# Optimization experiments

Measured on AMD Instinct MI355X. Metric: run time of the kernel, lower is better.

The kernel has to match this reference:

```python
import jax, jax.numpy as jnp
import numpy as np

B, T, D, H = 4, 2048, 1024, 16
DK = D // H

def setup_inputs() -> dict:
    key = jax.random.key(0)
    k1, k2, k3 = jax.random.split(key, 3)
    x = jax.random.normal(k1, (B, T, D), dtype=jnp.float32)
    w_qkv = jax.random.normal(k2, (D, 3 * D), dtype=jnp.float32) * (1.0 / np.sqrt(D))
    w_proj = jax.random.normal(k3, (D, D), dtype=jnp.float32) * (1.0 / np.sqrt(D))
    # additive causal mask: 0 on/below diagonal, -inf above
    neg = jnp.finfo(jnp.float32).min
    attn_mask = jnp.where(jnp.tril(jnp.ones((T, T), dtype=bool)), 0.0, neg)[None, None]
    return {"x": x, "attn_mask": attn_mask, "w_qkv": w_qkv, "w_proj": w_proj}


def reference(x, attn_mask, w_qkv, w_proj):
    Bx, Tx, Dx = x.shape
    qkv = x @ w_qkv                                  # [B,T,3D]
    q, k, v = jnp.split(qkv, 3, axis=-1)
    # [B,T,D] -> [B,H,T,dk]
    def to_heads(t):
        return t.reshape(Bx, Tx, H, DK).transpose(0, 2, 1, 3)
    q, k, v = to_heads(q), to_heads(k), to_heads(v)
    attn = jnp.einsum("bhqd,bhkd->bhqk", q, k) / jnp.sqrt(jnp.float32(DK))
    attn = attn + attn_mask
    attn = jax.nn.softmax(attn, axis=-1)
    out = jnp.einsum("bhqk,bhkd->bhqd", attn, v)     # [B,H,T,dk]
    out = out.transpose(0, 2, 1, 3).reshape(Bx, Tx, Dx)
    return out @ w_proj
```

## Files before the change

### kernel.cpp

```cpp
#include <hip/hip_runtime.h>
#include <hip/hip_bf16.h>
#include <stdint.h>

typedef __bf16 bf16x8 __attribute__((ext_vector_type(8)));
typedef __bf16 bf16x4 __attribute__((ext_vector_type(4)));
typedef float  f32x4  __attribute__((ext_vector_type(4)));

__device__ __forceinline__ void gl_lds16(const void* g, void* l) {
  __builtin_amdgcn_global_load_lds(
      (const __attribute__((address_space(1))) unsigned int*)g,
      (__attribute__((address_space(3))) unsigned int*)l, 16, 0, 0);
}

__global__ __launch_bounds__(256) void convert_x(
    const float* __restrict__ src, __bf16* __restrict__ dst) {
  const size_t i = ((size_t)blockIdx.x * 256 + threadIdx.x) * 8;
  float4 v0 = *reinterpret_cast<const float4*>(src + i);
  float4 v1 = *reinterpret_cast<const float4*>(src + i + 4);
  bf16x8 o;
  o[0] = (__bf16)v0.x; o[1] = (__bf16)v0.y; o[2] = (__bf16)v0.z; o[3] = (__bf16)v0.w;
  o[4] = (__bf16)v1.x; o[5] = (__bf16)v1.y; o[6] = (__bf16)v1.z; o[7] = (__bf16)v1.w;
  *reinterpret_cast<bf16x8*>(dst + i) = o;
}

__global__ __launch_bounds__(256) void transpose_convert(
    const float* __restrict__ src, __bf16* __restrict__ dst, int K, int N) {
  __shared__ __bf16 tile[64][65];
  const int n0 = blockIdx.x * 64, k0 = blockIdx.y * 64;
  const int t = threadIdx.x;
#pragma unroll
  for (int e = 0; e < 16; ++e) {
    int idx = e * 256 + t;
    int kk = idx >> 6, nn = idx & 63;
    tile[nn][kk] = (__bf16)src[(size_t)(k0 + kk) * N + n0 + nn];
  }
  __syncthreads();
#pragma unroll
  for (int e = 0; e < 16; ++e) {
    int idx = e * 256 + t;
    int nn = idx >> 6, kk = idx & 63;
    dst[(size_t)(n0 + nn) * K + k0 + kk] = tile[nn][kk];
  }
}

__global__ __launch_bounds__(256) void qkv_gemm(
    const __bf16* __restrict__ Xb, const __bf16* __restrict__ WT,
    __bf16* __restrict__ Qb, __bf16* __restrict__ Kb, __bf16* __restrict__ Vb) {
  __shared__ __bf16 As[128 * 32];
  __shared__ __bf16 Bs[128 * 32];
  const int t = threadIdx.x;
  const int l = t & 63, w = t >> 6;
  const int g = l >> 4, lr = l & 15;
  const int wm = w >> 1, wn = w & 1;
  const int lin = blockIdx.y * gridDim.x + blockIdx.x;
  const int cpx = (gridDim.x * gridDim.y) >> 3;
  const int swz = (lin & 7) * cpx + (lin >> 3);
  const int m0 = (swz / 24) * 128, n0 = (swz % 24) * 128;

  f32x4 acc[4][4] = {};

  for (int kb = 0; kb < 1024; kb += 32) {
#pragma unroll
    for (int rep = 0; rep < 2; ++rep) {
      int c = w * 128 + rep * 64 + l;
      int row = c >> 2, col = (c & 3) * 8;
      gl_lds16(Xb + (size_t)(m0 + row) * 1024 + kb + col,
               As + (size_t)(w * 128 + rep * 64) * 8);
      gl_lds16(WT + (size_t)(n0 + row) * 1024 + kb + col,
               Bs + (size_t)(w * 128 + rep * 64) * 8);
    }
    __syncthreads();

    bf16x8 a[4], b[4];
#pragma unroll
    for (int mf = 0; mf < 4; ++mf)
      a[mf] = *reinterpret_cast<bf16x8*>(&As[(wm * 64 + mf * 16 + lr) * 32 + g * 8]);
#pragma unroll
    for (int nf = 0; nf < 4; ++nf)
      b[nf] = *reinterpret_cast<bf16x8*>(&Bs[(wn * 64 + nf * 16 + lr) * 32 + g * 8]);
#pragma unroll
    for (int mf = 0; mf < 4; ++mf)
#pragma unroll
      for (int nf = 0; nf < 4; ++nf)
        acc[mf][nf] = __builtin_amdgcn_mfma_f32_16x16x32_bf16(
            a[mf], b[nf], acc[mf][nf], 0, 0, 0);
    __syncthreads();
  }

#pragma unroll
  for (int mf = 0; mf < 4; ++mf)
#pragma unroll
    for (int nf = 0; nf < 4; ++nf) {
      int m_ = m0 + wm * 64 + mf * 16 + g * 4;
      int n = n0 + wn * 64 + nf * 16 + lr;
      int which = n >> 10, hc = n & 1023;
      int hh = hc >> 6, dk = hc & 63;
      int bbv = m_ >> 11, tt = m_ & 2047;
      if (which == 2) {
        bf16x4 vk;
        vk[0] = (__bf16)acc[mf][nf][0]; vk[1] = (__bf16)acc[mf][nf][1];
        vk[2] = (__bf16)acc[mf][nf][2]; vk[3] = (__bf16)acc[mf][nf][3];
        *reinterpret_cast<bf16x4*>(
            &Vb[((size_t)(bbv * 16 + hh) * 64 + dk) * 2048 + tt]) = vk;
      } else {
#pragma unroll
        for (int j = 0; j < 4; ++j) {
          size_t off = (((size_t)(bbv * 16 + hh)) * 2048 + tt + j) * 64 + dk;
          float v = acc[mf][nf][j];
          if (which == 0) Qb[off] = (__bf16)(v * 0.18033688f);
          else            Kb[off] = (__bf16)v;
        }
      }
    }
}

__global__ __launch_bounds__(256, 2) void attn_kernel(
    const __bf16* __restrict__ Qb, const __bf16* __restrict__ Kb,
    const __bf16* __restrict__ VTb, __bf16* __restrict__ Ob) {
  __shared__ __bf16 Ks[2][4096];
  __shared__ __bf16 Vs[2][4096];
  __shared__ __bf16 PlA[4][1024];
  __shared__ __bf16 PlB[4][1024];
  const int t = threadIdx.x, l = t & 63, w = t >> 6;
  const int g = l >> 4, lr = l & 15;
  const int bid = blockIdx.x;
  const int logical = (bid & 7) * 64 + (bid >> 3);
  const int pj = logical & 7, bh = logical >> 3;
  const int bb = bh >> 4, h = bh & 15;
  const __bf16* Kbase = Kb  + (size_t)bh * 2048 * 64;
  const __bf16* Vbase = VTb + (size_t)bh * 64 * 2048;
  const __bf16* Qbase = Qb  + (size_t)bh * 2048 * 64;
  const int swz = (lr & 7) << 4;

  int cur = 0;
#pragma unroll 1
  for (int phase = 0; phase < 2; ++phase) {
    const int J = phase ? (15 - pj) : pj;
    const int qtA = 2 * J, qtB = 2 * J + 1;
    const int qrowA = J * 128 + w * 16 + lr;
    const int qrowB = qrowA + 64;
    const bf16x8 qfA0 = *reinterpret_cast<const bf16x8*>(Qbase + (size_t)qrowA * 64 + g * 8);
    const bf16x8 qfA1 = *reinterpret_cast<const bf16x8*>(Qbase + (size_t)qrowA * 64 + 32 + g * 8);
    const bf16x8 qfB0 = *reinterpret_cast<const bf16x8*>(Qbase + (size_t)qrowB * 64 + g * 8);
    const bf16x8 qfB1 = *reinterpret_cast<const bf16x8*>(Qbase + (size_t)qrowB * 64 + 32 + g * 8);

    f32x4 otA[4] = {}, otB[4] = {};
    float lsA = 0.f, lsB = 0.f;

#pragma unroll
    for (int rep = 0; rep < 2; ++rep) {
      int c = w * 128 + rep * 64 + l;
      int row = c >> 3, cc = c & 7;
      int pc = (cc ^ (row & 7)) * 8;
      gl_lds16(Kbase + (size_t)row * 64 + pc, &Ks[cur][(w * 128 + rep * 64) * 8]);
      gl_lds16(Vbase + (size_t)row * 2048 + pc, &Vs[cur][(w * 128 + rep * 64) * 8]);
    }
    __syncthreads();

    for (int kt = 0; kt <= qtB; ++kt) {
      const bool aAct = (kt <= qtA);
      if (kt < qtB) {
        const int nv0 = (kt + 1) * 64;
#pragma unroll
        for (int rep = 0; rep < 2; ++rep) {
          int c = w * 128 + rep * 64 + l;
          int row = c >> 3, cc = c & 7;
          int pc = (cc ^ (row & 7)) * 8;
          gl_lds16(Kbase + (size_t)(nv0 + row) * 64 + pc,
                   &Ks[cur ^ 1][(w * 128 + rep * 64) * 8]);
          gl_lds16(Vbase + (size_t)row * 2048 + nv0 + pc,
                   &Vs[cur ^ 1][(w * 128 + rep * 64) * 8]);
        }
      }
      bf16x8 klo[4], khi[4];
#pragma unroll
      for (int nf = 0; nf < 4; ++nf) {
        const char* kr = (const char*)&Ks[cur][(nf * 16 + lr) * 64];
        klo[nf] = *reinterpret_cast<const bf16x8*>(kr + ((g * 16) ^ swz));
        khi[nf] = *reinterpret_cast<const bf16x8*>(kr + ((64 + g * 16) ^ swz));
      }
      f32x4 stA[4], stB[4];
      __builtin_amdgcn_s_setprio(1);
#pragma unroll
      for (int nf = 0; nf < 4; ++nf) {
        f32x4 z = {};
        z = __builtin_amdgcn_mfma_f32_16x16x32_bf16(klo[nf], qfB0, z, 0, 0, 0);
        stB[nf] = __builtin_amdgcn_mfma_f32_16x16x32_bf16(khi[nf], qfB1, z, 0, 0, 0);
      }
      if (aAct) {
#pragma unroll
        for (int nf = 0; nf < 4; ++nf) {
          f32x4 z = {};
          z = __builtin_amdgcn_mfma_f32_16x16x32_bf16(klo[nf], qfA0, z, 0, 0, 0);
          stA[nf] = __builtin_amdgcn_mfma_f32_16x16x32_bf16(khi[nf], qfA1, z, 0, 0, 0);
        }
      }
      __builtin_amdgcn_s_setprio(0);
      if (kt == qtB) {
#pragma unroll
        for (int nf = 0; nf < 4; ++nf)
#pragma unroll
          for (int j = 0; j < 4; ++j)
            if (nf * 16 + g * 4 + j > w * 16 + lr) stB[nf][j] = -INFINITY;
      }
      if (aAct && kt == qtA) {
#pragma unroll
        for (int nf = 0; nf < 4; ++nf)
#pragma unroll
          for (int j = 0; j < 4; ++j)
            if (nf * 16 + g * 4 + j > w * 16 + lr) stA[nf][j] = -INFINITY;
      }
      {
        float rs = 0.f;
        char* prow = (char*)&PlB[w][lr * 64];
#pragma unroll
        for (int nf = 0; nf < 4; ++nf) {
#pragma unroll
          for (int j = 0; j < 4; ++j) {
            float p = __builtin_amdgcn_exp2f(stB[nf][j]);
            stB[nf][j] = p;
            rs += p;
          }
          bf16x4 pk;
          pk[0] = (__bf16)stB[nf][0]; pk[1] = (__bf16)stB[nf][1];
          pk[2] = (__bf16)stB[nf][2]; pk[3] = (__bf16)stB[nf][3];
          *reinterpret_cast<bf16x4*>(prow + ((nf * 32 + g * 8) ^ swz)) = pk;
        }
        lsB += rs;
      }
      if (aAct) {
        float rs = 0.f;
        char* prow = (char*)&PlA[w][lr * 64];
#pragma unroll
        for (int nf = 0; nf < 4; ++nf) {
#pragma unroll
          for (int j = 0; j < 4; ++j) {
            float p = __builtin_amdgcn_exp2f(stA[nf][j]);
            stA[nf][j] = p;
            rs += p;
          }
          bf16x4 pk;
          pk[0] = (__bf16)stA[nf][0]; pk[1] = (__bf16)stA[nf][1];
          pk[2] = (__bf16)stA[nf][2]; pk[3] = (__bf16)stA[nf][3];
          *reinterpret_cast<bf16x4*>(prow + ((nf * 32 + g * 8) ^ swz)) = pk;
        }
        lsA += rs;
      }
      {
        bf16x8 vlo[4], vhi[4];
#pragma unroll
        for (int nf = 0; nf < 4; ++nf) {
          const char* vr = (const char*)&Vs[cur][(nf * 16 + lr) * 64];
          vlo[nf] = *reinterpret_cast<const bf16x8*>(vr + ((g * 16) ^ swz));
          vhi[nf] = *reinterpret_cast<const bf16x8*>(vr + ((64 + g * 16) ^ swz));
        }
        const char* prB = (const char*)&PlB[w][lr * 64];
        bf16x8 pb0 = *reinterpret_cast<const bf16x8*>(prB + ((g * 16) ^ swz));
        bf16x8 pb1 = *reinterpret_cast<const bf16x8*>(prB + ((64 + g * 16) ^ swz));
        __builtin_amdgcn_s_setprio(1);
#pragma unroll
        for (int nf = 0; nf < 4; ++nf) {
          otB[nf] = __builtin_amdgcn_mfma_f32_16x16x32_bf16(vlo[nf], pb0, otB[nf], 0, 0, 0);
          otB[nf] = __builtin_amdgcn_mfma_f32_16x16x32_bf16(vhi[nf], pb1, otB[nf], 0, 0, 0);
        }
        __builtin_amdgcn_s_setprio(0);
        if (aAct) {
          const char* prA = (const char*)&PlA[w][lr * 64];
          bf16x8 pa0 = *reinterpret_cast<const bf16x8*>(prA + ((g * 16) ^ swz));
          bf16x8 pa1 = *reinterpret_cast<const bf16x8*>(prA + ((64 + g * 16) ^ swz));
          __builtin_amdgcn_s_setprio(1);
#pragma unroll
          for (int nf = 0; nf < 4; ++nf) {
            otA[nf] = __builtin_amdgcn_mfma_f32_16x16x32_bf16(vlo[nf], pa0, otA[nf], 0, 0, 0);
            otA[nf] = __builtin_amdgcn_mfma_f32_16x16x32_bf16(vhi[nf], pa1, otA[nf], 0, 0, 0);
          }
          __builtin_amdgcn_s_setprio(0);
        }
      }
      __syncthreads();
      cur ^= 1;
    }

    lsA += __shfl_xor(lsA, 16); lsA += __shfl_xor(lsA, 32);
    lsB += __shfl_xor(lsB, 16); lsB += __shfl_xor(lsB, 32);
    const float rlA = 1.f / lsA, rlB = 1.f / lsB;
#pragma unroll
    for (int nf = 0; nf < 4; ++nf) {
      bf16x4 ok;
      ok[0] = (__bf16)(otA[nf][0] * rlA); ok[1] = (__bf16)(otA[nf][1] * rlA);
      ok[2] = (__bf16)(otA[nf][2] * rlA); ok[3] = (__bf16)(otA[nf][3] * rlA);
      *reinterpret_cast<bf16x4*>(
          &Ob[((size_t)(bb * 2048 + qrowA)) * 1024 + h * 64 + nf * 16 + g * 4]) = ok;
      bf16x4 ok2;
      ok2[0] = (__bf16)(otB[nf][0] * rlB); ok2[1] = (__bf16)(otB[nf][1] * rlB);
      ok2[2] = (__bf16)(otB[nf][2] * rlB); ok2[3] = (__bf16)(otB[nf][3] * rlB);
      *reinterpret_cast<bf16x4*>(
          &Ob[((size_t)(bb * 2048 + qrowB)) * 1024 + h * 64 + nf * 16 + g * 4]) = ok2;
    }
  }
}

__global__ __launch_bounds__(256) void proj_gemm(
    const __bf16* __restrict__ A, const __bf16* __restrict__ WT,
    float* __restrict__ Out) {
  __shared__ __bf16 As[128 * 32];
  __shared__ __bf16 Bs[128 * 32];
  const int t = threadIdx.x;
  const int l = t & 63, w = t >> 6;
  const int g = l >> 4, lr = l & 15;
  const int wm = w >> 1, wn = w & 1;
  const int lin = blockIdx.y * gridDim.x + blockIdx.x;
  const int cpx = (gridDim.x * gridDim.y) >> 3;
  const int swz = (lin & 7) * cpx + (lin >> 3);
  const int m0 = (swz >> 3) * 128, n0 = (swz & 7) * 128;

  f32x4 acc[4][4] = {};

  for (int kb = 0; kb < 1024; kb += 32) {
#pragma unroll
    for (int rep = 0; rep < 2; ++rep) {
      int c = w * 128 + rep * 64 + l;
      int row = c >> 2, col = (c & 3) * 8;
      gl_lds16(A + (size_t)(m0 + row) * 1024 + kb + col,
               As + (size_t)(w * 128 + rep * 64) * 8);
      gl_lds16(WT + (size_t)(n0 + row) * 1024 + kb + col,
               Bs + (size_t)(w * 128 + rep * 64) * 8);
    }
    __syncthreads();

    bf16x8 a[4], b[4];
#pragma unroll
    for (int mf = 0; mf < 4; ++mf)
      a[mf] = *reinterpret_cast<bf16x8*>(&As[(wm * 64 + mf * 16 + lr) * 32 + g * 8]);
#pragma unroll
    for (int nf = 0; nf < 4; ++nf)
      b[nf] = *reinterpret_cast<bf16x8*>(&Bs[(wn * 64 + nf * 16 + lr) * 32 + g * 8]);
#pragma unroll
    for (int mf = 0; mf < 4; ++mf)
#pragma unroll
      for (int nf = 0; nf < 4; ++nf)
        acc[mf][nf] = __builtin_amdgcn_mfma_f32_16x16x32_bf16(
            a[mf], b[nf], acc[mf][nf], 0, 0, 0);
    __syncthreads();
  }

#pragma unroll
  for (int mf = 0; mf < 4; ++mf)
#pragma unroll
    for (int nf = 0; nf < 4; ++nf)
#pragma unroll
      for (int j = 0; j < 4; ++j) {
        int m = m0 + wm * 64 + mf * 16 + g * 4 + j;
        int n = n0 + wn * 64 + nf * 16 + lr;
        Out[(size_t)m * 1024 + n] = acc[mf][nf][j];
      }
}

extern "C" void kernel_launch(void* const* d_in, const int* in_sizes, int n_in,
                              void* d_out, int out_size, void* d_ws, size_t ws_size,
                              hipStream_t stream) {
  const float* x      = (const float*)d_in[0];
  const float* w_qkv  = (const float*)d_in[2];
  const float* w_proj = (const float*)d_in[3];
  float* out = (float*)d_out;

  char* ws = (char*)d_ws;
  __bf16* wt_qkv  = (__bf16*)(ws);
  __bf16* wt_proj = (__bf16*)(ws + 6291456);
  __bf16* Qb      = (__bf16*)(ws + 8388608);
  __bf16* Kb      = (__bf16*)(ws + 8388608 + 16777216);
  __bf16* VTb     = (__bf16*)(ws + 8388608 + 2 * 16777216);
  __bf16* Ob      = (__bf16*)(ws + 8388608 + 3 * 16777216);
  __bf16* Xb      = Ob;

  convert_x<<<4096, 256, 0, stream>>>(x, Xb);
  transpose_convert<<<dim3(3072 / 64, 1024 / 64), 256, 0, stream>>>(w_qkv, wt_qkv, 1024, 3072);
  transpose_convert<<<dim3(1024 / 64, 1024 / 64), 256, 0, stream>>>(w_proj, wt_proj, 1024, 1024);
  qkv_gemm<<<dim3(24, 64), 256, 0, stream>>>(Xb, wt_qkv, Qb, Kb, VTb);
  attn_kernel<<<512, 256, 0, stream>>>(Qb, Kb, VTb, Ob);
  proj_gemm<<<dim3(8, 64), 256, 0, stream>>>(Ob, wt_proj, out);
}
```

Baseline: 172.6 us.

## Rewrite QKV and projection GEMMs with shared triple-buffered swizzled 128x256 core

Replaces both GEMM kernels with a shared core that uses 128x256 tiles, a three-stage LDS ring of async global-to-LDS loads with explicit vmcnt waits and one barrier per K step, and XOR-swizzled LDS columns to avoid bank conflicts. Each wave now computes a 128x64 strip, and MFMA issue priority is raised. The aim is to hide global load latency and cut barrier and LDS-conflict overhead, at the cost of more registers and LDS per block and fewer blocks in the grid.

```diff
diff --git a/kernel.cpp b/kernel.cpp
--- a/kernel.cpp
+++ b/kernel.cpp
@@ -43,74 +43,158 @@
   }
 }
 
-__global__ __launch_bounds__(256) void qkv_gemm(
-    const __bf16* __restrict__ Xb, const __bf16* __restrict__ WT,
-    __bf16* __restrict__ Qb, __bf16* __restrict__ Kb, __bf16* __restrict__ Vb) {
-  __shared__ __bf16 As[128 * 32];
-  __shared__ __bf16 Bs[128 * 32];
-  const int t = threadIdx.x;
-  const int l = t & 63, w = t >> 6;
-  const int g = l >> 4, lr = l & 15;
-  const int wm = w >> 1, wn = w & 1;
-  const int lin = blockIdx.y * gridDim.x + blockIdx.x;
-  const int cpx = (gridDim.x * gridDim.y) >> 3;
-  const int swz = (lin & 7) * cpx + (lin >> 3);
-  const int m0 = (swz / 24) * 128, n0 = (swz % 24) * 128;
-
-  f32x4 acc[4][4] = {};
-
-  for (int kb = 0; kb < 1024; kb += 32) {
-#pragma unroll
-    for (int rep = 0; rep < 2; ++rep) {
-      int c = w * 128 + rep * 64 + l;
-      int row = c >> 2, col = (c & 3) * 8;
-      gl_lds16(Xb + (size_t)(m0 + row) * 1024 + kb + col,
-               As + (size_t)(w * 128 + rep * 64) * 8);
-      gl_lds16(WT + (size_t)(n0 + row) * 1024 + kb + col,
-               Bs + (size_t)(w * 128 + rep * 64) * 8);
-    }
-    __syncthreads();
-
-    bf16x8 a[4], b[4];
-#pragma unroll
-    for (int mf = 0; mf < 4; ++mf)
-      a[mf] = *reinterpret_cast<bf16x8*>(&As[(wm * 64 + mf * 16 + lr) * 32 + g * 8]);
+__device__ __forceinline__ void gemm_core_1024(
+    const __bf16* __restrict__ Ag, const __bf16* __restrict__ Bg,
+    int m0, int n0, __bf16* lds, f32x4 (&acc)[8][4]) {
+  const int tid = threadIdx.x;
+  const int wv = tid >> 6, l = tid & 63, g = l >> 4, lr = l & 15;
+  const int sswL = (lr & 3) ^ ((lr >> 2) & 3);
+
+  int arow[2], acol[2], brow[4], bcol[4];
+#pragma unroll
+  for (int e = 0; e < 2; ++e) {
+    int c = e * 256 + tid, row = c >> 2, slot = c & 3;
+    arow[e] = row;
+    acol[e] = (slot ^ ((row & 3) ^ ((row >> 2) & 3))) * 8;
+  }
+#pragma unroll
+  for (int e = 0; e < 4; ++e) {
+    int c = e * 256 + tid, row = c >> 2, slot = c & 3;
+    brow[e] = row;
+    bcol[e] = (slot ^ ((row & 3) ^ ((row >> 2) & 3))) * 8;
+  }
+
+  auto STAGE = [&](int bufb, int t) {
+    const int kb = t * 32;
+#pragma unroll
+    for (int e = 0; e < 2; ++e)
+      gl_lds16(Ag + (size_t)(m0 + arow[e]) * 1024 + kb + acol[e],
+               lds + bufb + (e * 256 + wv * 64) * 8);
+#pragma unroll
+    for (int e = 0; e < 4; ++e)
+      gl_lds16(Bg + (size_t)(n0 + brow[e]) * 1024 + kb + bcol[e],
+               lds + bufb + 4096 + (e * 256 + wv * 64) * 8);
+  };
+
+  int cur = 0, nx = 12288, nn = 24576;
+  STAGE(cur, 0);
+  STAGE(nx, 1);
+
+#pragma unroll 1
+  for (int t = 0; t < 32; ++t) {
+    if (t < 31) asm volatile("s_waitcnt vmcnt(6)" ::: "memory");
+    else        asm volatile("s_waitcnt vmcnt(0)" ::: "memory");
+    __builtin_amdgcn_s_barrier();
+    __builtin_amdgcn_sched_barrier(0);
+    if (t + 2 < 32) STAGE(nn, t + 2);
+
+    const char* Ab = (const char*)(lds + cur);
+    const char* Bb = (const char*)(lds + cur + 4096);
+    bf16x8 a[8], b[4];
+#pragma unroll
+    for (int mf = 0; mf < 8; ++mf)
+      a[mf] = *reinterpret_cast<const bf16x8*>(
+          Ab + (mf * 16 + lr) * 64 + ((g ^ sswL) << 4));
 #pragma unroll
     for (int nf = 0; nf < 4; ++nf)
-      b[nf] = *reinterpret_cast<bf16x8*>(&Bs[(wn * 64 + nf * 16 + lr) * 32 + g * 8]);
-#pragma unroll
-    for (int mf = 0; mf < 4; ++mf)
+      b[nf] = *reinterpret_cast<const bf16x8*>(
+          Bb + (wv * 64 + nf * 16 + lr) * 64 + ((g ^ sswL) << 4));
+    __builtin_amdgcn_s_setprio(1);
+#pragma unroll
+    for (int mf = 0; mf < 8; ++mf)
 #pragma unroll
       for (int nf = 0; nf < 4; ++nf)
         acc[mf][nf] = __builtin_amdgcn_mfma_f32_16x16x32_bf16(
             a[mf], b[nf], acc[mf][nf], 0, 0, 0);
-    __syncthreads();
-  }
-
-#pragma unroll
-  for (int mf = 0; mf < 4; ++mf)
-#pragma unroll
-    for (int nf = 0; nf < 4; ++nf) {
-      int m_ = m0 + wm * 64 + mf * 16 + g * 4;
-      int n = n0 + wn * 64 + nf * 16 + lr;
-      int which = n >> 10, hc = n & 1023;
-      int hh = hc >> 6, dk = hc & 63;
-      int bbv = m_ >> 11, tt = m_ & 2047;
-      if (which == 2) {
+    __builtin_amdgcn_s_setprio(0);
+
+    int tmp = cur; cur = nx; nx = nn; nn = tmp;
+  }
+}
+
+__global__ __launch_bounds__(256, 2) void qkv_gemm(
+    const __bf16* __restrict__ Xb, const __bf16* __restrict__ WT,
+    __bf16* __restrict__ Qb, __bf16* __restrict__ Kb, __bf16* __restrict__ Vb) {
+  __shared__ __bf16 lds[36864];
+  const int lin = blockIdx.x;
+  const int sw = (lin & 7) * 96 + (lin >> 3);
+  const int rb = sw / 12, cb = sw % 12;
+  const int m0 = rb * 128, n0 = cb * 256;
+
+  f32x4 acc[8][4] = {};
+  gemm_core_1024(Xb, WT, m0, n0, lds, acc);
+
+  const int tid = threadIdx.x, wv = tid >> 6, l = tid & 63, g = l >> 4, lr = l & 15;
+  const int which = cb >> 2;
+
+  if (which == 2) {
+#pragma unroll
+    for (int mf = 0; mf < 8; ++mf)
+#pragma unroll
+      for (int nf = 0; nf < 4; ++nf) {
+        int m_ = m0 + mf * 16 + g * 4;
+        int n  = n0 + wv * 64 + nf * 16 + lr;
+        int hc = n & 1023, hh = hc >> 6, dk = hc & 63;
+        int bbv = m_ >> 11, tt = m_ & 2047;
         bf16x4 vk;
         vk[0] = (__bf16)acc[mf][nf][0]; vk[1] = (__bf16)acc[mf][nf][1];
         vk[2] = (__bf16)acc[mf][nf][2]; vk[3] = (__bf16)acc[mf][nf][3];
         *reinterpret_cast<bf16x4*>(
             &Vb[((size_t)(bbv * 16 + hh) * 64 + dk) * 2048 + tt]) = vk;
-      } else {
-#pragma unroll
-        for (int j = 0; j < 4; ++j) {
-          size_t off = (((size_t)(bbv * 16 + hh)) * 2048 + tt + j) * 64 + dk;
-          float v = acc[mf][nf][j];
-          if (which == 0) Qb[off] = (__bf16)(v * 0.18033688f);
-          else            Kb[off] = (__bf16)v;
-        }
-      }
+      }
+  } else if (which == 0) {
+#pragma unroll
+    for (int mf = 0; mf < 8; ++mf)
+#pragma unroll
+      for (int nf = 0; nf < 4; ++nf) {
+        int m_ = m0 + mf * 16 + g * 4;
+        int n  = n0 + wv * 64 + nf * 16 + lr;
+        int hc = n & 1023, hh = hc >> 6, dk = hc & 63;
+        int bbv = m_ >> 11, tt = m_ & 2047;
+#pragma unroll
+        for (int j = 0; j < 4; ++j)
+          Qb[(((size_t)(bbv * 16 + hh)) * 2048 + tt + j) * 64 + dk] =
+              (__bf16)(acc[mf][nf][j] * 0.18033688f);
+      }
+  } else {
+#pragma unroll
+    for (int mf = 0; mf < 8; ++mf)
+#pragma unroll
+      for (int nf = 0; nf < 4; ++nf) {
+        int m_ = m0 + mf * 16 + g * 4;
+        int n  = n0 + wv * 64 + nf * 16 + lr;
+        int hc = n & 1023, hh = hc >> 6, dk = hc & 63;
+        int bbv = m_ >> 11, tt = m_ & 2047;
+#pragma unroll
+        for (int j = 0; j < 4; ++j)
+          Kb[(((size_t)(bbv * 16 + hh)) * 2048 + tt + j) * 64 + dk] =
+              (__bf16)acc[mf][nf][j];
+      }
+  }
+}
+
+__global__ __launch_bounds__(256, 2) void proj_gemm(
+    const __bf16* __restrict__ A, const __bf16* __restrict__ WT,
+    float* __restrict__ Out) {
+  __shared__ __bf16 lds[36864];
+  const int lin = blockIdx.x;
+  const int sw = (lin & 7) * 32 + (lin >> 3);
+  const int rb = sw >> 2, cb = sw & 3;
+  const int m0 = rb * 128, n0 = cb * 256;
+
+  f32x4 acc[8][4] = {};
+  gemm_core_1024(A, WT, m0, n0, lds, acc);
+
+  const int tid = threadIdx.x, wv = tid >> 6, l = tid & 63, g = l >> 4, lr = l & 15;
+#pragma unroll
+  for (int mf = 0; mf < 8; ++mf)
+#pragma unroll
+    for (int nf = 0; nf < 4; ++nf) {
+      int m_ = m0 + mf * 16 + g * 4;
+      int n  = n0 + wv * 64 + nf * 16 + lr;
+#pragma unroll
+      for (int j = 0; j < 4; ++j)
+        Out[(size_t)(m_ + j) * 1024 + n] = acc[mf][nf][j];
     }
 }
 
@@ -300,62 +384,6 @@
   }
 }
 
-__global__ __launch_bounds__(256) void proj_gemm(
-    const __bf16* __restrict__ A, const __bf16* __restrict__ WT,
-    float* __restrict__ Out) {
-  __shared__ __bf16 As[128 * 32];
-  __shared__ __bf16 Bs[128 * 32];
-  const int t = threadIdx.x;
-  const int l = t & 63, w = t >> 6;
-  const int g = l >> 4, lr = l & 15;
-  const int wm = w >> 1, wn = w & 1;
-  const int lin = blockIdx.y * gridDim.x + blockIdx.x;
-  const int cpx = (gridDim.x * gridDim.y) >> 3;
-  const int swz = (lin & 7) * cpx + (lin >> 3);
-  const int m0 = (swz >> 3) * 128, n0 = (swz & 7) * 128;
-
-  f32x4 acc[4][4] = {};
-
-  for (int kb = 0; kb < 1024; kb += 32) {
-#pragma unroll
-    for (int rep = 0; rep < 2; ++rep) {
-      int c = w * 128 + rep * 64 + l;
-      int row = c >> 2, col = (c & 3) * 8;
-      gl_lds16(A + (size_t)(m0 + row) * 1024 + kb + col,
-               As + (size_t)(w * 128 + rep * 64) * 8);
-      gl_lds16(WT + (size_t)(n0 + row) * 1024 + kb + col,
-               Bs + (size_t)(w * 128 + rep * 64) * 8);
-    }
-    __syncthreads();
-
-    bf16x8 a[4], b[4];
-#pragma unroll
-    for (int mf = 0; mf < 4; ++mf)
-      a[mf] = *reinterpret_cast<bf16x8*>(&As[(wm * 64 + mf * 16 + lr) * 32 + g * 8]);
-#pragma unroll
-    for (int nf = 0; nf < 4; ++nf)
-      b[nf] = *reinterpret_cast<bf16x8*>(&Bs[(wn * 64 + nf * 16 + lr) * 32 + g * 8]);
-#pragma unroll
-    for (int mf = 0; mf < 4; ++mf)
-#pragma unroll
-      for (int nf = 0; nf < 4; ++nf)
-        acc[mf][nf] = __builtin_amdgcn_mfma_f32_16x16x32_bf16(
-            a[mf], b[nf], acc[mf][nf], 0, 0, 0);
-    __syncthreads();
-  }
-
-#pragma unroll
-  for (int mf = 0; mf < 4; ++mf)
-#pragma unroll
-    for (int nf = 0; nf < 4; ++nf)
-#pragma unroll
-      for (int j = 0; j < 4; ++j) {
-        int m = m0 + wm * 64 + mf * 16 + g * 4 + j;
-        int n = n0 + wn * 64 + nf * 16 + lr;
-        Out[(size_t)m * 1024 + n] = acc[mf][nf][j];
-      }
-}
-
 extern "C" void kernel_launch(void* const* d_in, const int* in_sizes, int n_in,
                               void* d_out, int out_size, void* d_ws, size_t ws_size,
                               hipStream_t stream) {
@@ -376,7 +404,7 @@
   convert_x<<<4096, 256, 0, stream>>>(x, Xb);
   transpose_convert<<<dim3(3072 / 64, 1024 / 64), 256, 0, stream>>>(w_qkv, wt_qkv, 1024, 3072);
   transpose_convert<<<dim3(1024 / 64, 1024 / 64), 256, 0, stream>>>(w_proj, wt_proj, 1024, 1024);
-  qkv_gemm<<<dim3(24, 64), 256, 0, stream>>>(Xb, wt_qkv, Qb, Kb, VTb);
+  qkv_gemm<<<768, 256, 0, stream>>>(Xb, wt_qkv, Qb, Kb, VTb);
   attn_kernel<<<512, 256, 0, stream>>>(Qb, Kb, VTb, Ob);
-  proj_gemm<<<dim3(8, 64), 256, 0, stream>>>(Ob, wt_proj, out);
-}
+  proj_gemm<<<256, 256, 0, stream>>>(Ob, wt_proj, out);
+}
```

After: 163.5 us. 5.3% less time.
